# Optimization experiments

Measured on AMD Instinct MI355X. Metric: run time of the kernel, lower is better.

## Reference

```python
import jax, jax.numpy as jnp
import numpy as np

D_MODEL = 1024
NHEAD = 16
HEAD_DIM = D_MODEL // NHEAD
EPS = 1e-6


def setup_inputs() -> dict:
    key = jax.random.key(0)
    ks = jax.random.split(key, 9)
    B, S = 2, 2048
    scale = 1.0 / np.sqrt(D_MODEL)
    inp = {
        "x": jax.random.normal(ks[0], (B, S, D_MODEL), dtype=jnp.float32),
        "wq": jax.random.normal(ks[1], (D_MODEL, D_MODEL), dtype=jnp.float32) * scale,
        "bq": jnp.zeros((D_MODEL,), dtype=jnp.float32),
        "wk": jax.random.normal(ks[2], (D_MODEL, D_MODEL), dtype=jnp.float32) * scale,
        "bk": jnp.zeros((D_MODEL,), dtype=jnp.float32),
        "wv": jax.random.normal(ks[3], (D_MODEL, D_MODEL), dtype=jnp.float32) * scale,
        "bv": jnp.zeros((D_MODEL,), dtype=jnp.float32),
        "wo": jax.random.normal(ks[4], (D_MODEL, D_MODEL), dtype=jnp.float32) * scale,
        "bo": jnp.zeros((D_MODEL,), dtype=jnp.float32),
    }
    return inp


def _split_heads(x):
    B, S, _ = x.shape
    return x.reshape(B, S, NHEAD, HEAD_DIM).transpose(0, 2, 1, 3)  # [B,H,S,Dh]


def reference(x, wq, bq, wk, bk, wv, bv, wo, bo):
    # projections (torch Linear: x @ W^T + b)
    q = _split_heads(x @ wq.T + bq)
    k = _split_heads(x @ wk.T + bk)
    v = _split_heads(x @ wv.T + bv)
    # positive feature map: elu(x) + 1
    q_feat = jax.nn.elu(q) + 1.0
    k_feat = jax.nn.elu(k) + 1.0
    # dense O(n^2) kernelized scores, per original module
    scores = jnp.einsum('bhid,bhjd->bhij', q_feat, k_feat)
    denom = jnp.maximum(scores.sum(axis=-1, keepdims=True), EPS)
    weights = scores / denom  # dropout p=0 -> identity
    attended = jnp.einsum('bhij,bhjd->bhid', weights, v)
    B, H, S, Dh = attended.shape
    merged = attended.transpose(0, 2, 1, 3).reshape(B, S, H * Dh)
    return merged @ wo.T + bo
```

## Files before the change

kernel.cpp:

```cpp
#include <hip/hip_runtime.h>
#include <math.h>

#define S_LEN 2048
#define BATCH 2
#define DM 1024
#define NH 16
#define DH 64
#define EPS 1e-6f
#define LDSP 68

typedef __attribute__((ext_vector_type(8))) short bf16x8;
typedef __attribute__((ext_vector_type(4))) float f32x4;

__device__ __forceinline__ unsigned short f2bf(float f) {
    unsigned u = __float_as_uint(f);
    u = (u + 0x7fffu + ((u >> 16) & 1u)) >> 16;
    return (unsigned short)u;
}
__device__ __forceinline__ float2 bf2f2(unsigned u) {
    float2 r;
    r.x = __uint_as_float(u << 16);
    r.y = __uint_as_float(u & 0xFFFF0000u);
    return r;
}
__device__ __forceinline__ void load16(const void* g, void* l) {
    __builtin_amdgcn_global_load_lds(
        (const __attribute__((address_space(1))) unsigned int*)g,
        (__attribute__((address_space(3))) unsigned int*)l,
        16, 0, 0);
}

__global__ __launch_bounds__(256) void cvt5_bf16(
    const float* __restrict__ s0, const float* __restrict__ s1,
    const float* __restrict__ s2, const float* __restrict__ s3,
    const float* __restrict__ s4,
    unsigned short* __restrict__ d0, unsigned short* __restrict__ d1,
    unsigned short* __restrict__ d2, unsigned short* __restrict__ d3,
    unsigned short* __restrict__ d4,
    int n8_x, int n8_w)
{
    const int z = blockIdx.y;
    const float* s = (z == 0) ? s0 : (z == 1) ? s1 : (z == 2) ? s2 : (z == 3) ? s3 : s4;
    unsigned short* d = (z == 0) ? d0 : (z == 1) ? d1 : (z == 2) ? d2 : (z == 3) ? d3 : d4;
    const int n8 = (z == 0) ? n8_x : n8_w;
    int i = blockIdx.x * 256 + threadIdx.x;
    if (i >= n8) return;
    float4 a = ((const float4*)s)[2 * i];
    float4 b = ((const float4*)s)[2 * i + 1];
    uint4 o;
    o.x = (unsigned)f2bf(a.x) | ((unsigned)f2bf(a.y) << 16);
    o.y = (unsigned)f2bf(a.z) | ((unsigned)f2bf(a.w) << 16);
    o.z = (unsigned)f2bf(b.x) | ((unsigned)f2bf(b.y) << 16);
    o.w = (unsigned)f2bf(b.z) | ((unsigned)f2bf(b.w) << 16);
    ((uint4*)d)[i] = o;
}

template <int OUTF32>
__global__ __launch_bounds__(256) void gemm_mfma(
    const unsigned short* __restrict__ A,
    const unsigned short* __restrict__ W0, const unsigned short* __restrict__ W1,
    const unsigned short* __restrict__ W2,
    const float* __restrict__ B0, const float* __restrict__ B1, const float* __restrict__ B2,
    void* __restrict__ O0, void* __restrict__ O1, void* __restrict__ O2,
    int M, int N, int K, int act_mask)
{
    const int z = blockIdx.z;
    const unsigned short* W = (z == 0) ? W0 : (z == 1) ? W1 : W2;
    const float* bias       = (z == 0) ? B0 : (z == 1) ? B1 : B2;
    void* O                 = (z == 0) ? O0 : (z == 1) ? O1 : O2;
    const bool act = (act_mask >> z) & 1;

    __shared__ __align__(16) unsigned short AsU[128 * 32];
    __shared__ __align__(16) unsigned short BsU[128 * 32];

    const int tid = threadIdx.x;
    const int wave = tid >> 6;
    const int lane = tid & 63;
    const int quad = lane >> 4;
    const int lm = lane & 15;
    const int wr = wave >> 1, wc = wave & 1;

    const int rowBase = blockIdx.y * 128;
    const int colBase = blockIdx.x * 128;

    const int s0 = wave * 128 + lane, s1 = s0 + 64;
    const int ra0 = s0 >> 2, ca0 = (s0 & 3) ^ ((ra0 >> 1) & 3);
    const int ra1 = s1 >> 2, ca1 = (s1 & 3) ^ ((ra1 >> 1) & 3);
    const unsigned short* Ag0 = A + (size_t)(rowBase + ra0) * K + ca0 * 8;
    const unsigned short* Ag1 = A + (size_t)(rowBase + ra1) * K + ca1 * 8;
    const unsigned short* Wg0 = W + (size_t)(colBase + ra0) * K + ca0 * 8;
    const unsigned short* Wg1 = W + (size_t)(colBase + ra1) * K + ca1 * 8;
    unsigned short* lA0 = AsU + (size_t)(wave * 128) * 8;
    unsigned short* lA1 = AsU + (size_t)(wave * 128 + 64) * 8;
    unsigned short* lB0 = BsU + (size_t)(wave * 128) * 8;
    unsigned short* lB1 = BsU + (size_t)(wave * 128 + 64) * 8;

    const unsigned short* pA[4];
    const unsigned short* pB[4];
#pragma unroll
    for (int i = 0; i < 4; ++i) {
        int r = wr * 64 + i * 16 + lm;
        int cp = quad ^ ((r >> 1) & 3);
        pA[i] = AsU + (size_t)(r * 4 + cp) * 8;
        int n = wc * 64 + i * 16 + lm;
        int cq = quad ^ ((n >> 1) & 3);
        pB[i] = BsU + (size_t)(n * 4 + cq) * 8;
    }

    f32x4 acc[4][4];
#pragma unroll
    for (int i = 0; i < 4; ++i)
#pragma unroll
        for (int j = 0; j < 4; ++j)
            acc[i][j] = (f32x4){0.f, 0.f, 0.f, 0.f};

    for (int k0 = 0; k0 < K; k0 += 32) {
        load16(Ag0 + k0, lA0);
        load16(Ag1 + k0, lA1);
        load16(Wg0 + k0, lB0);
        load16(Wg1 + k0, lB1);
        __syncthreads();
        bf16x8 aF[4], bF[4];
#pragma unroll
        for (int i = 0; i < 4; ++i) {
            aF[i] = *(const bf16x8*)pA[i];
            bF[i] = *(const bf16x8*)pB[i];
        }
#pragma unroll
        for (int i = 0; i < 4; ++i)
#pragma unroll
            for (int j = 0; j < 4; ++j)
                acc[i][j] = __builtin_amdgcn_mfma_f32_16x16x32_bf16(aF[i], bF[j], acc[i][j], 0, 0, 0);
        __syncthreads();
    }

#pragma unroll
    for (int j = 0; j < 4; ++j) {
        const int col = colBase + wc * 64 + j * 16 + lm;
        const float bc = bias[col];
#pragma unroll
        for (int i = 0; i < 4; ++i) {
            const int row0 = rowBase + wr * 64 + i * 16 + quad * 4;
#pragma unroll
            for (int reg = 0; reg < 4; ++reg) {
                float v = acc[i][j][reg] + bc;
                if (act) v = (v > 0.0f) ? (v + 1.0f) : __expf(v);
                size_t idx = (size_t)(row0 + reg) * N + col;
                if (OUTF32) ((float*)O)[idx] = v;
                else ((unsigned short*)O)[idx] = f2bf(v);
            }
        }
    }
}

__global__ __launch_bounds__(256) void kv_kernel(
    const unsigned short* __restrict__ kf, const unsigned short* __restrict__ vv,
    float* __restrict__ kv, float* __restrict__ ksum)
{
    const int bh = blockIdx.x;
    const int b = bh >> 4, h = bh & 15;
    const int posBase = blockIdx.y * 128;

    __shared__ __align__(16) float Ks[32][LDSP];
    __shared__ __align__(16) float Vs[32][LDSP];

    const int tid = threadIdx.x;
    const int ty = tid >> 4, tx = tid & 15;
    const int r0 = ty * 4, c0 = tx * 4;
    const int p = tid >> 3;
    const int f0 = (tid & 7) * 8;

    float acc[4][4] = {};
    float srow[4] = {};

    for (int t = 0; t < 4; ++t) {
        size_t g = ((size_t)(b * S_LEN + posBase + t * 32 + p)) * DM + h * DH + f0;
        uint4 kq = *(const uint4*)(kf + g);
        uint4 vq = *(const uint4*)(vv + g);
        float2 k0v = bf2f2(kq.x), k1v = bf2f2(kq.y), k2v = bf2f2(kq.z), k3v = bf2f2(kq.w);
        float2 v0v = bf2f2(vq.x), v1v = bf2f2(vq.y), v2v = bf2f2(vq.z), v3v = bf2f2(vq.w);
        *(float4*)&Ks[p][f0]     = make_float4(k0v.x, k0v.y, k1v.x, k1v.y);
        *(float4*)&Ks[p][f0 + 4] = make_float4(k2v.x, k2v.y, k3v.x, k3v.y);
        *(float4*)&Vs[p][f0]     = make_float4(v0v.x, v0v.y, v1v.x, v1v.y);
        *(float4*)&Vs[p][f0 + 4] = make_float4(v2v.x, v2v.y, v3v.x, v3v.y);
        __syncthreads();
#pragma unroll
        for (int q = 0; q < 32; ++q) {
            float4 a = *(const float4*)&Ks[q][r0];
            float4 bv = *(const float4*)&Vs[q][c0];
            float aa[4] = {a.x, a.y, a.z, a.w};
            float bb[4] = {bv.x, bv.y, bv.z, bv.w};
#pragma unroll
            for (int i = 0; i < 4; ++i)
#pragma unroll
                for (int j = 0; j < 4; ++j)
                    acc[i][j] += aa[i] * bb[j];
            if (tx == 0) {
                srow[0] += aa[0]; srow[1] += aa[1];
                srow[2] += aa[2]; srow[3] += aa[3];
            }
        }
        __syncthreads();
    }
    float* kvp = kv + (size_t)bh * DH * DH;
#pragma unroll
    for (int i = 0; i < 4; ++i)
#pragma unroll
        for (int j = 0; j < 4; ++j)
            atomicAdd(&kvp[(r0 + i) * DH + c0 + j], acc[i][j]);
    if (tx == 0) {
#pragma unroll
        for (int i = 0; i < 4; ++i) atomicAdd(&ksum[bh * DH + r0 + i], srow[i]);
    }
}

__global__ __launch_bounds__(256) void attend_kernel(
    const unsigned short* __restrict__ qf, const float* __restrict__ kv,
    const float* __restrict__ ksum, unsigned short* __restrict__ att)
{
    const int sBase = blockIdx.x * 64;
    const int h = blockIdx.y;
    const int b = blockIdx.z;
    const int bh = b * NH + h;

    __shared__ __align__(16) float Qs[DH][LDSP];
    __shared__ __align__(16) float KVs[DH][LDSP];
    __shared__ __align__(16) float ks_s[DH];
    __shared__ float den_s[64];

    const int tid = threadIdx.x;
#pragma unroll
    for (int i = 0; i < 2; ++i) {
        int l = tid + 256 * i;
        int r = l >> 3;
        int f0 = (l & 7) * 8;
        size_t g = ((size_t)(b * S_LEN + sBase + r)) * DM + h * DH + f0;
        uint4 q4 = *(const uint4*)(qf + g);
        float2 a0 = bf2f2(q4.x), a1 = bf2f2(q4.y), a2 = bf2f2(q4.z), a3 = bf2f2(q4.w);
        Qs[f0 + 0][r] = a0.x; Qs[f0 + 1][r] = a0.y;
        Qs[f0 + 2][r] = a1.x; Qs[f0 + 3][r] = a1.y;
        Qs[f0 + 4][r] = a2.x; Qs[f0 + 5][r] = a2.y;
        Qs[f0 + 6][r] = a3.x; Qs[f0 + 7][r] = a3.y;
    }
#pragma unroll
    for (int i = 0; i < 4; ++i) {
        int l = tid + 256 * i;
        int r = l >> 4;
        int f0 = (l & 15) * 4;
        float4 kv4 = *(const float4*)(kv + (size_t)bh * DH * DH + r * DH + f0);
        *(float4*)&KVs[r][f0] = kv4;
    }
    if (tid < 16) {
        float4 s4 = *(const float4*)(ksum + bh * DH + tid * 4);
        *(float4*)&ks_s[tid * 4] = s4;
    }
    __syncthreads();
    if (tid < 64) {
        float d = 0.f;
#pragma unroll
        for (int f = 0; f < DH; ++f) d += Qs[f][tid] * ks_s[f];
        den_s[tid] = fmaxf(d, EPS);
    }
    __syncthreads();

    const int ty = tid >> 4, tx = tid & 15;
    const int r0 = ty * 4, c0 = tx * 4;
    float acc[4][4] = {};
#pragma unroll 8
    for (int f = 0; f < DH; ++f) {
        float4 a = *(const float4*)&Qs[f][r0];
        float4 bv = *(const float4*)&KVs[f][c0];
        float aa[4] = {a.x, a.y, a.z, a.w};
        float bb[4] = {bv.x, bv.y, bv.z, bv.w};
#pragma unroll
        for (int i = 0; i < 4; ++i)
#pragma unroll
            for (int j = 0; j < 4; ++j)
                acc[i][j] += aa[i] * bb[j];
    }
#pragma unroll
    for (int i = 0; i < 4; ++i) {
        float inv = 1.0f / den_s[r0 + i];
        ushort4 o;
        o.x = f2bf(acc[i][0] * inv);
        o.y = f2bf(acc[i][1] * inv);
        o.z = f2bf(acc[i][2] * inv);
        o.w = f2bf(acc[i][3] * inv);
        size_t g = ((size_t)(b * S_LEN + sBase + r0 + i)) * DM + h * DH + c0;
        *(ushort4*)&att[g] = o;
    }
}

extern "C" void kernel_launch(void* const* d_in, const int* in_sizes, int n_in,
                              void* d_out, int out_size, void* d_ws, size_t ws_size,
                              hipStream_t stream) {
    const float* x  = (const float*)d_in[0];
    const float* wq = (const float*)d_in[1];
    const float* bq = (const float*)d_in[2];
    const float* wk = (const float*)d_in[3];
    const float* bk = (const float*)d_in[4];
    const float* wv = (const float*)d_in[5];
    const float* bv = (const float*)d_in[6];
    const float* wo = (const float*)d_in[7];
    const float* bo = (const float*)d_in[8];
    float* out = (float*)d_out;

    const size_t ND  = (size_t)BATCH * S_LEN * DM;
    const size_t NDW = (size_t)DM * DM;

    unsigned short* x_bf  = (unsigned short*)d_ws;
    unsigned short* wq_bf = x_bf + ND;
    unsigned short* wk_bf = wq_bf + NDW;
    unsigned short* wv_bf = wk_bf + NDW;
    unsigned short* wo_bf = wv_bf + NDW;
    unsigned short* qf_bf = wo_bf + NDW;
    unsigned short* kf_bf = qf_bf + ND;
    unsigned short* vv_bf = kf_bf + ND;
    unsigned short* att_bf = vv_bf + ND;
    float* kvb  = (float*)(att_bf + ND);
    float* ksum = kvb + (size_t)BATCH * NH * DH * DH;

    const int M = BATCH * S_LEN;
    const int n8x = (int)(ND / 8), n8w = (int)(NDW / 8);

    cvt5_bf16<<<dim3(n8x / 256, 5), 256, 0, stream>>>(
        x, wq, wk, wv, wo, x_bf, wq_bf, wk_bf, wv_bf, wo_bf, n8x, n8w);

    gemm_mfma<0><<<dim3(DM / 128, M / 128, 3), 256, 0, stream>>>(
        x_bf, wq_bf, wk_bf, wv_bf, bq, bk, bv,
        (void*)qf_bf, (void*)kf_bf, (void*)vv_bf, M, DM, DM, 0b011);

    hipMemsetAsync(kvb, 0,
                   ((size_t)BATCH * NH * DH * DH + (size_t)BATCH * NH * DH) * sizeof(float),
                   stream);

    kv_kernel<<<dim3(BATCH * NH, S_LEN / 128), 256, 0, stream>>>(kf_bf, vv_bf, kvb, ksum);

    attend_kernel<<<dim3(S_LEN / 64, NH, BATCH), 256, 0, stream>>>(qf_bf, kvb, ksum, att_bf);

    gemm_mfma<1><<<dim3(DM / 128, M / 128, 1), 256, 0, stream>>>(
        att_bf, wo_bf, wo_bf, wo_bf, bo, bo, bo,
        (void*)out, (void*)out, (void*)out, M, DM, DM, 0);
}
```

Baseline: 208.8 us.

## Replace atomic KV accumulation with partial sums plus reduce, MFMA attend

KV outer products are computed per wave into per-position-block partial buffers, removing the memset and global atomics, then a reduce kernel sums them into a transposed bf16 KV matrix and ksum. The attend step now uses bf16 MFMA with swizzled LDS tiles loaded via global_load_lds instead of scalar FP32 FMA. This adds one extra kernel launch and extra workspace traffic for partials, and rounds KV to bf16, which lowers precision.

Measured after the change: 191.3 us. -8.4%, faster.

```diff
diff --git a/kernel.cpp b/kernel.cpp
--- a/kernel.cpp
+++ b/kernel.cpp
@@ -7,7 +7,6 @@
 #define NH 16
 #define DH 64
 #define EPS 1e-6f
-#define LDSP 68
 
 typedef __attribute__((ext_vector_type(8))) short bf16x8;
 typedef __attribute__((ext_vector_type(4))) float f32x4;
@@ -22,6 +21,11 @@
     r.x = __uint_as_float(u << 16);
     r.y = __uint_as_float(u & 0xFFFF0000u);
     return r;
+}
+__device__ __forceinline__ void unpack8(uint4 u, float* f) {
+    float2 a = bf2f2(u.x), b = bf2f2(u.y), c = bf2f2(u.z), d = bf2f2(u.w);
+    f[0] = a.x; f[1] = a.y; f[2] = b.x; f[3] = b.y;
+    f[4] = c.x; f[5] = c.y; f[6] = d.x; f[7] = d.y;
 }
 __device__ __forceinline__ void load16(const void* g, void* l) {
     __builtin_amdgcn_global_load_lds(
@@ -153,141 +157,222 @@
     }
 }
 
-__global__ __launch_bounds__(256) void kv_kernel(
+__global__ __launch_bounds__(256) void kv_part_kernel(
     const unsigned short* __restrict__ kf, const unsigned short* __restrict__ vv,
-    float* __restrict__ kv, float* __restrict__ ksum)
+    float* __restrict__ kv_part, float* __restrict__ ksum_part)
 {
     const int bh = blockIdx.x;
     const int b = bh >> 4, h = bh & 15;
-    const int posBase = blockIdx.y * 128;
-
-    __shared__ __align__(16) float Ks[32][LDSP];
-    __shared__ __align__(16) float Vs[32][LDSP];
-
     const int tid = threadIdx.x;
-    const int ty = tid >> 4, tx = tid & 15;
-    const int r0 = ty * 4, c0 = tx * 4;
-    const int p = tid >> 3;
-    const int f0 = (tid & 7) * 8;
-
-    float acc[4][4] = {};
-    float srow[4] = {};
-
-    for (int t = 0; t < 4; ++t) {
-        size_t g = ((size_t)(b * S_LEN + posBase + t * 32 + p)) * DM + h * DH + f0;
-        uint4 kq = *(const uint4*)(kf + g);
-        uint4 vq = *(const uint4*)(vv + g);
-        float2 k0v = bf2f2(kq.x), k1v = bf2f2(kq.y), k2v = bf2f2(kq.z), k3v = bf2f2(kq.w);
-        float2 v0v = bf2f2(vq.x), v1v = bf2f2(vq.y), v2v = bf2f2(vq.z), v3v = bf2f2(vq.w);
-        *(float4*)&Ks[p][f0]     = make_float4(k0v.x, k0v.y, k1v.x, k1v.y);
-        *(float4*)&Ks[p][f0 + 4] = make_float4(k2v.x, k2v.y, k3v.x, k3v.y);
-        *(float4*)&Vs[p][f0]     = make_float4(v0v.x, v0v.y, v1v.x, v1v.y);
-        *(float4*)&Vs[p][f0 + 4] = make_float4(v2v.x, v2v.y, v3v.x, v3v.y);
-        __syncthreads();
-#pragma unroll
-        for (int q = 0; q < 32; ++q) {
-            float4 a = *(const float4*)&Ks[q][r0];
-            float4 bv = *(const float4*)&Vs[q][c0];
-            float aa[4] = {a.x, a.y, a.z, a.w};
-            float bb[4] = {bv.x, bv.y, bv.z, bv.w};
-#pragma unroll
-            for (int i = 0; i < 4; ++i)
-#pragma unroll
-                for (int j = 0; j < 4; ++j)
+    const int wave = tid >> 6, lane = tid & 63;
+    const int p = blockIdx.y * 4 + wave;
+    const int posBase = p * 128;
+
+    __shared__ __align__(16) float Ks[4][2][16][68];
+    __shared__ __align__(16) float Vs[4][2][16][68];
+
+    const int pos_l = lane >> 3;
+    const int f0 = (lane & 7) * 8;
+    const int r0 = pos_l * 8;
+    const int c0 = f0;
+
+    float acc[8][8] = {};
+    float srow[8] = {};
+
+    for (int st = 0; st < 8; ++st) {
+        const int buf = st & 1;
+        size_t g0 = ((size_t)(b * S_LEN + posBase + st * 16 + pos_l)) * DM + h * DH + f0;
+        size_t g1 = g0 + (size_t)8 * DM;
+        uint4 ka = *(const uint4*)(kf + g0);
+        uint4 kb = *(const uint4*)(kf + g1);
+        uint4 va = *(const uint4*)(vv + g0);
+        uint4 vb = *(const uint4*)(vv + g1);
+        float kaf[8], kbf[8], vaf[8], vbf[8];
+        unpack8(ka, kaf); unpack8(kb, kbf); unpack8(va, vaf); unpack8(vb, vbf);
+#pragma unroll
+        for (int j = 0; j < 8; ++j) srow[j] += kaf[j] + kbf[j];
+        *(float4*)&Ks[wave][buf][pos_l][f0]         = make_float4(kaf[0], kaf[1], kaf[2], kaf[3]);
+        *(float4*)&Ks[wave][buf][pos_l][f0 + 4]     = make_float4(kaf[4], kaf[5], kaf[6], kaf[7]);
+        *(float4*)&Ks[wave][buf][pos_l + 8][f0]     = make_float4(kbf[0], kbf[1], kbf[2], kbf[3]);
+        *(float4*)&Ks[wave][buf][pos_l + 8][f0 + 4] = make_float4(kbf[4], kbf[5], kbf[6], kbf[7]);
+        *(float4*)&Vs[wave][buf][pos_l][f0]         = make_float4(vaf[0], vaf[1], vaf[2], vaf[3]);
+        *(float4*)&Vs[wave][buf][pos_l][f0 + 4]     = make_float4(vaf[4], vaf[5], vaf[6], vaf[7]);
+        *(float4*)&Vs[wave][buf][pos_l + 8][f0]     = make_float4(vbf[0], vbf[1], vbf[2], vbf[3]);
+        *(float4*)&Vs[wave][buf][pos_l + 8][f0 + 4] = make_float4(vbf[4], vbf[5], vbf[6], vbf[7]);
+#pragma unroll 4
+        for (int q = 0; q < 16; ++q) {
+            float4 a0 = *(const float4*)&Ks[wave][buf][q][r0];
+            float4 a1 = *(const float4*)&Ks[wave][buf][q][r0 + 4];
+            float4 b0 = *(const float4*)&Vs[wave][buf][q][c0];
+            float4 b1 = *(const float4*)&Vs[wave][buf][q][c0 + 4];
+            float aa[8] = {a0.x, a0.y, a0.z, a0.w, a1.x, a1.y, a1.z, a1.w};
+            float bb[8] = {b0.x, b0.y, b0.z, b0.w, b1.x, b1.y, b1.z, b1.w};
+#pragma unroll
+            for (int i = 0; i < 8; ++i)
+#pragma unroll
+                for (int j = 0; j < 8; ++j)
                     acc[i][j] += aa[i] * bb[j];
-            if (tx == 0) {
-                srow[0] += aa[0]; srow[1] += aa[1];
-                srow[2] += aa[2]; srow[3] += aa[3];
-            }
-        }
-        __syncthreads();
-    }
-    float* kvp = kv + (size_t)bh * DH * DH;
-#pragma unroll
-    for (int i = 0; i < 4; ++i)
-#pragma unroll
-        for (int j = 0; j < 4; ++j)
-            atomicAdd(&kvp[(r0 + i) * DH + c0 + j], acc[i][j]);
-    if (tx == 0) {
-#pragma unroll
-        for (int i = 0; i < 4; ++i) atomicAdd(&ksum[bh * DH + r0 + i], srow[i]);
-    }
-}
-
-__global__ __launch_bounds__(256) void attend_kernel(
-    const unsigned short* __restrict__ qf, const float* __restrict__ kv,
+        }
+    }
+
+#pragma unroll
+    for (int j = 0; j < 8; ++j) {
+        srow[j] += __shfl_xor(srow[j], 8);
+        srow[j] += __shfl_xor(srow[j], 16);
+        srow[j] += __shfl_xor(srow[j], 32);
+    }
+
+    float* kvp = kv_part + ((size_t)bh * 16 + p) * (DH * DH);
+#pragma unroll
+    for (int j = 0; j < 8; ++j) {
+        *(float4*)&kvp[(c0 + j) * DH + r0] =
+            make_float4(acc[0][j], acc[1][j], acc[2][j], acc[3][j]);
+        *(float4*)&kvp[(c0 + j) * DH + r0 + 4] =
+            make_float4(acc[4][j], acc[5][j], acc[6][j], acc[7][j]);
+    }
+    if (pos_l == 0) {
+        float* ksp = ksum_part + ((size_t)bh * 16 + p) * DH + f0;
+        *(float4*)&ksp[0] = make_float4(srow[0], srow[1], srow[2], srow[3]);
+        *(float4*)&ksp[4] = make_float4(srow[4], srow[5], srow[6], srow[7]);
+    }
+}
+
+__global__ __launch_bounds__(256) void kv_reduce_kernel(
+    const float* __restrict__ kv_part, const float* __restrict__ ksum_part,
+    unsigned short* __restrict__ kvT_bf, float* __restrict__ ksum)
+{
+    const int bh = blockIdx.x;
+    const int tid = threadIdx.x;
+    float s[16] = {};
+    const float* base = kv_part + (size_t)bh * 16 * (DH * DH) + tid * 16;
+#pragma unroll 4
+    for (int p = 0; p < 16; ++p) {
+        const float4* b4 = (const float4*)(base + (size_t)p * (DH * DH));
+#pragma unroll
+        for (int q = 0; q < 4; ++q) {
+            float4 v = b4[q];
+            s[q * 4 + 0] += v.x; s[q * 4 + 1] += v.y;
+            s[q * 4 + 2] += v.z; s[q * 4 + 3] += v.w;
+        }
+    }
+    unsigned short us[16];
+#pragma unroll
+    for (int i = 0; i < 16; ++i) us[i] = f2bf(s[i]);
+    uint4 o0, o1;
+    o0.x = (unsigned)us[0]  | ((unsigned)us[1]  << 16);
+    o0.y = (unsigned)us[2]  | ((unsigned)us[3]  << 16);
+    o0.z = (unsigned)us[4]  | ((unsigned)us[5]  << 16);
+    o0.w = (unsigned)us[6]  | ((unsigned)us[7]  << 16);
+    o1.x = (unsigned)us[8]  | ((unsigned)us[9]  << 16);
+    o1.y = (unsigned)us[10] | ((unsigned)us[11] << 16);
+    o1.z = (unsigned)us[12] | ((unsigned)us[13] << 16);
+    o1.w = (unsigned)us[14] | ((unsigned)us[15] << 16);
+    uint4* dst = (uint4*)(kvT_bf + (size_t)bh * (DH * DH) + tid * 16);
+    dst[0] = o0; dst[1] = o1;
+    if (tid < DH) {
+        float t = 0.f;
+#pragma unroll 4
+        for (int p = 0; p < 16; ++p)
+            t += ksum_part[((size_t)bh * 16 + p) * DH + tid];
+        ksum[bh * DH + tid] = t;
+    }
+}
+
+__global__ __launch_bounds__(256) void attend_mfma(
+    const unsigned short* __restrict__ qf, const unsigned short* __restrict__ kvT_bf,
     const float* __restrict__ ksum, unsigned short* __restrict__ att)
 {
-    const int sBase = blockIdx.x * 64;
-    const int h = blockIdx.y;
-    const int b = blockIdx.z;
-    const int bh = b * NH + h;
-
-    __shared__ __align__(16) float Qs[DH][LDSP];
-    __shared__ __align__(16) float KVs[DH][LDSP];
+    const int sBase = blockIdx.x * 128;
+    const int bh = blockIdx.y;
+    const int b = bh >> 4, h = bh & 15;
+
+    __shared__ __align__(16) unsigned short Qs[128 * 64];
+    __shared__ __align__(16) unsigned short Ts[64 * 64];
     __shared__ __align__(16) float ks_s[DH];
-    __shared__ float den_s[64];
+    __shared__ float den_s[128];
 
     const int tid = threadIdx.x;
+    const int wave = tid >> 6, lane = tid & 63;
+    const int quad = lane >> 4, lm = lane & 15;
+
+#pragma unroll
+    for (int i = 0; i < 4; ++i) {
+        int slot = (wave * 4 + i) * 64 + lane;
+        int r = slot >> 3;
+        int c = (slot & 7) ^ (r & 7);
+        const unsigned short* src =
+            qf + ((size_t)(b * S_LEN + sBase + r)) * DM + h * DH + c * 8;
+        load16(src, Qs + (size_t)(wave * 4 + i) * 512);
+    }
 #pragma unroll
     for (int i = 0; i < 2; ++i) {
-        int l = tid + 256 * i;
-        int r = l >> 3;
-        int f0 = (l & 7) * 8;
-        size_t g = ((size_t)(b * S_LEN + sBase + r)) * DM + h * DH + f0;
-        uint4 q4 = *(const uint4*)(qf + g);
-        float2 a0 = bf2f2(q4.x), a1 = bf2f2(q4.y), a2 = bf2f2(q4.z), a3 = bf2f2(q4.w);
-        Qs[f0 + 0][r] = a0.x; Qs[f0 + 1][r] = a0.y;
-        Qs[f0 + 2][r] = a1.x; Qs[f0 + 3][r] = a1.y;
-        Qs[f0 + 4][r] = a2.x; Qs[f0 + 5][r] = a2.y;
-        Qs[f0 + 6][r] = a3.x; Qs[f0 + 7][r] = a3.y;
-    }
-#pragma unroll
-    for (int i = 0; i < 4; ++i) {
-        int l = tid + 256 * i;
-        int r = l >> 4;
-        int f0 = (l & 15) * 4;
-        float4 kv4 = *(const float4*)(kv + (size_t)bh * DH * DH + r * DH + f0);
-        *(float4*)&KVs[r][f0] = kv4;
-    }
-    if (tid < 16) {
-        float4 s4 = *(const float4*)(ksum + bh * DH + tid * 4);
-        *(float4*)&ks_s[tid * 4] = s4;
-    }
+        int slot = (wave * 2 + i) * 64 + lane;
+        int e = slot >> 3;
+        int c = (slot & 7) ^ (e & 7);
+        const unsigned short* src = kvT_bf + (size_t)bh * (DH * DH) + e * DH + c * 8;
+        load16(src, Ts + (size_t)(wave * 2 + i) * 512);
+    }
+    if (tid < 16)
+        *(float4*)&ks_s[tid * 4] = *(const float4*)&ksum[bh * DH + tid * 4];
     __syncthreads();
-    if (tid < 64) {
+
+    if (tid < 128) {
+        const int r = tid;
         float d = 0.f;
 #pragma unroll
-        for (int f = 0; f < DH; ++f) d += Qs[f][tid] * ks_s[f];
-        den_s[tid] = fmaxf(d, EPS);
+        for (int cxx = 0; cxx < 8; ++cxx) {
+            int slot = r * 8 + (cxx ^ (r & 7));
+            uint4 u = *(const uint4*)(Qs + slot * 8);
+            float f[8]; unpack8(u, f);
+            const float* kss = &ks_s[cxx * 8];
+#pragma unroll
+            for (int j = 0; j < 8; ++j) d += f[j] * kss[j];
+        }
+        den_s[r] = fmaxf(d, EPS);
     }
     __syncthreads();
 
-    const int ty = tid >> 4, tx = tid & 15;
-    const int r0 = ty * 4, c0 = tx * 4;
-    float acc[4][4] = {};
-#pragma unroll 8
-    for (int f = 0; f < DH; ++f) {
-        float4 a = *(const float4*)&Qs[f][r0];
-        float4 bv = *(const float4*)&KVs[f][c0];
-        float aa[4] = {a.x, a.y, a.z, a.w};
-        float bb[4] = {bv.x, bv.y, bv.z, bv.w};
-#pragma unroll
-        for (int i = 0; i < 4; ++i)
-#pragma unroll
-            for (int j = 0; j < 4; ++j)
-                acc[i][j] += aa[i] * bb[j];
-    }
-#pragma unroll
-    for (int i = 0; i < 4; ++i) {
-        float inv = 1.0f / den_s[r0 + i];
-        ushort4 o;
-        o.x = f2bf(acc[i][0] * inv);
-        o.y = f2bf(acc[i][1] * inv);
-        o.z = f2bf(acc[i][2] * inv);
-        o.w = f2bf(acc[i][3] * inv);
-        size_t g = ((size_t)(b * S_LEN + sBase + r0 + i)) * DM + h * DH + c0;
-        *(ushort4*)&att[g] = o;
+    f32x4 acc[2][4];
+#pragma unroll
+    for (int ti = 0; ti < 2; ++ti)
+#pragma unroll
+        for (int tj = 0; tj < 4; ++tj)
+            acc[ti][tj] = (f32x4){0.f, 0.f, 0.f, 0.f};
+
+#pragma unroll
+    for (int ks_i = 0; ks_i < 2; ++ks_i) {
+        bf16x8 aF[2], bF[4];
+#pragma unroll
+        for (int ti = 0; ti < 2; ++ti) {
+            int r = wave * 32 + ti * 16 + lm;
+            int cx = (ks_i * 4 + quad) ^ (r & 7);
+            aF[ti] = *(const bf16x8*)(Qs + (r * 8 + cx) * 8);
+        }
+#pragma unroll
+        for (int tj = 0; tj < 4; ++tj) {
+            int e = tj * 16 + lm;
+            int cx = (ks_i * 4 + quad) ^ (e & 7);
+            bF[tj] = *(const bf16x8*)(Ts + (e * 8 + cx) * 8);
+        }
+#pragma unroll
+        for (int ti = 0; ti < 2; ++ti)
+#pragma unroll
+            for (int tj = 0; tj < 4; ++tj)
+                acc[ti][tj] = __builtin_amdgcn_mfma_f32_16x16x32_bf16(aF[ti], bF[tj], acc[ti][tj], 0, 0, 0);
+    }
+
+#pragma unroll
+    for (int ti = 0; ti < 2; ++ti) {
+        const int rloc0 = wave * 32 + ti * 16 + quad * 4;
+#pragma unroll
+        for (int reg = 0; reg < 4; ++reg) {
+            float inv = 1.0f / den_s[rloc0 + reg];
+            unsigned short* dst =
+                att + ((size_t)(b * S_LEN + sBase + rloc0 + reg)) * DM + h * DH;
+#pragma unroll
+            for (int tj = 0; tj < 4; ++tj)
+                dst[tj * 16 + lm] = f2bf(acc[ti][tj][reg] * inv);
+        }
     }
 }
 
@@ -307,18 +392,21 @@
 
     const size_t ND  = (size_t)BATCH * S_LEN * DM;
     const size_t NDW = (size_t)DM * DM;
-
-    unsigned short* x_bf  = (unsigned short*)d_ws;
-    unsigned short* wq_bf = x_bf + ND;
-    unsigned short* wk_bf = wq_bf + NDW;
-    unsigned short* wv_bf = wk_bf + NDW;
-    unsigned short* wo_bf = wv_bf + NDW;
-    unsigned short* qf_bf = wo_bf + NDW;
-    unsigned short* kf_bf = qf_bf + ND;
-    unsigned short* vv_bf = kf_bf + ND;
+    const int BH = BATCH * NH;
+
+    unsigned short* x_bf   = (unsigned short*)d_ws;
+    unsigned short* wq_bf  = x_bf + ND;
+    unsigned short* wk_bf  = wq_bf + NDW;
+    unsigned short* wv_bf  = wk_bf + NDW;
+    unsigned short* wo_bf  = wv_bf + NDW;
+    unsigned short* qf_bf  = wo_bf + NDW;
+    unsigned short* kf_bf  = qf_bf + ND;
+    unsigned short* vv_bf  = kf_bf + ND;
     unsigned short* att_bf = vv_bf + ND;
-    float* kvb  = (float*)(att_bf + ND);
-    float* ksum = kvb + (size_t)BATCH * NH * DH * DH;
+    unsigned short* kvT_bf = att_bf + ND;
+    float* kv_part   = (float*)(kvT_bf + (size_t)BH * DH * DH);
+    float* ksum_part = kv_part + (size_t)BH * 16 * DH * DH;
+    float* ksum      = ksum_part + (size_t)BH * 16 * DH;
 
     const int M = BATCH * S_LEN;
     const int n8x = (int)(ND / 8), n8w = (int)(NDW / 8);
@@ -330,13 +418,11 @@
         x_bf, wq_bf, wk_bf, wv_bf, bq, bk, bv,
         (void*)qf_bf, (void*)kf_bf, (void*)vv_bf, M, DM, DM, 0b011);
 
-    hipMemsetAsync(kvb, 0,
-                   ((size_t)BATCH * NH * DH * DH + (size_t)BATCH * NH * DH) * sizeof(float),
-                   stream);
-
-    kv_kernel<<<dim3(BATCH * NH, S_LEN / 128), 256, 0, stream>>>(kf_bf, vv_bf, kvb, ksum);
-
-    attend_kernel<<<dim3(S_LEN / 64, NH, BATCH), 256, 0, stream>>>(qf_bf, kvb, ksum, att_bf);
+    kv_part_kernel<<<dim3(BH, 4), 256, 0, stream>>>(kf_bf, vv_bf, kv_part, ksum_part);
+
+    kv_reduce_kernel<<<BH, 256, 0, stream>>>(kv_part, ksum_part, kvT_bf, ksum);
+
+    attend_mfma<<<dim3(S_LEN / 128, BH), 256, 0, stream>>>(qf_bf, kvT_bf, ksum, att_bf);
 
     gemm_mfma<1><<<dim3(DM / 128, M / 128, 1), 256, 0, stream>>>(
         att_bf, wo_bf, wo_bf, wo_bf, bo, bo, bo,
```
